# Kernel tuning notes

Hardware: AMD Instinct MI355X
Metric: run time of the kernel (lower is better)

## Reference

```python
import jax, jax.numpy as jnp
import numpy as np

B, L, D = 4, 2048, 1024
E, K, H = 8, 2, 4096
EPS = 1e-5


def setup_inputs() -> dict:
    key = jax.random.key(0)
    ks = jax.random.split(key, 6)
    x = jax.random.normal(ks[0], (B, L, D), jnp.float32)
    gate_w = jax.random.normal(ks[1], (E, D), jnp.float32) * 0.02
    W1 = jax.random.normal(ks[2], (E, D, H), jnp.float32) * 0.02
    b1 = jnp.zeros((E, H), jnp.float32)
    W2 = jax.random.normal(ks[3], (E, H, D), jnp.float32) * 0.02
    b2 = jnp.zeros((E, D), jnp.float32)
    gamma = jnp.ones((D,), jnp.float32)
    beta = jnp.zeros((D,), jnp.float32)
    return {"x": x, "gamma": gamma, "beta": beta, "gate_w": gate_w,
            "W1": W1, "b1": b1, "W2": W2, "b2": b2}


def reference(x, gamma, beta, gate_w, W1, b1, W2, b2):
    # LayerNorm (biased variance, eps=1e-5, matches torch.nn.LayerNorm)
    mu = jnp.mean(x, axis=-1, keepdims=True)
    var = jnp.mean((x - mu) ** 2, axis=-1, keepdims=True)
    xn = (x - mu) / jnp.sqrt(var + EPS) * gamma + beta
    xf = xn.reshape(-1, D)  # (T, D), T = B*L
    T = xf.shape[0]

    # gating: top-k logits -> softmax -> scatter into dense gates (T, E)
    logits = xf @ gate_w.T  # (T, E)
    top_v, top_i = jax.lax.top_k(logits, K)
    top_g = jax.nn.softmax(top_v, axis=-1)
    gates = jnp.zeros_like(logits).at[jnp.arange(T)[:, None], top_i].set(top_g)

    # experts: dense-equivalent of masked gather/FFN/scatter-add combine.
    # Non-selected experts contribute with gate weight 0 -> identical math.
    h = jax.nn.gelu(jnp.einsum('td,edh->teh', xf, W1) + b1, approximate=False)
    y = jnp.einsum('teh,ehd->ted', h, W2) + b2  # (T, E, D)
    out = jnp.einsum('te,ted->td', gates, y).reshape(B, L, D) + x

    # load-balance loss: MSE(mean gate per expert, uniform)
    load = jnp.mean(gates, axis=0)
    bal_loss = jnp.mean((load - 1.0 / E) ** 2)
    return out, bal_loss
```

## Files before the change

kernel.cpp:

```cpp
#include <hip/hip_runtime.h>
#include <hip/hip_bf16.h>

#define T_TOK 8192
#define DD 1024
#define EE 8
#define HH 4096
#define NA (2 * T_TOK)
#define NBLK (NA / 256)

typedef __bf16 bf16_t;
typedef __bf16 bf16x8 __attribute__((ext_vector_type(8)));
typedef __bf16 bf16x4 __attribute__((ext_vector_type(4)));
typedef float f32x4 __attribute__((ext_vector_type(4)));
typedef int   i32x4 __attribute__((ext_vector_type(4)));

union frag_u { i32x4 i; bf16x8 b; };

#define GLDS(g, l) __builtin_amdgcn_global_load_lds( \
    (const __attribute__((address_space(1))) void*)(g), \
    (__attribute__((address_space(3))) void*)(l), 16, 0, 0)

#define DSR(d, a)      asm volatile("ds_read_b128 %0, %1"           : "=v"(d) : "v"(a))
#define DSRO(d, a, O)  asm volatile("ds_read_b128 %0, %1 offset:" O : "=v"(d) : "v"(a))

#define VMW(N) asm volatile("s_waitcnt vmcnt(" #N ")" ::: "memory")

__device__ __forceinline__ float gelu_fast(float v) {
    float u = v * (0.79788456080286536f + 0.035677408136300125f * v * v);
    float a = 2.8853900817779268f * u;
    a = fminf(fmaxf(a, -87.0f), 87.0f);
    float t = __builtin_amdgcn_exp2f(a);
    return v * t * __builtin_amdgcn_rcpf(t + 1.0f);
}

__global__ __launch_bounds__(256) void ln_gate_kernel(
    const float* __restrict__ x, const float* __restrict__ gamma,
    const float* __restrict__ beta, const float* __restrict__ gate_w,
    bf16_t* __restrict__ xn, int* __restrict__ tokexp, float* __restrict__ tokgate)
{
    const int t = blockIdx.x;
    const int tid = threadIdx.x;
    const int lane = tid & 63, wave = tid >> 6;
    __shared__ float wred[4];
    __shared__ float stats[2];
    __shared__ float lred[32];
    __shared__ float logitsS[8];

    float4 v = ((const float4*)(x + (size_t)t * DD))[tid];
    float s = v.x + v.y + v.z + v.w;
#pragma unroll
    for (int o = 32; o > 0; o >>= 1) s += __shfl_down(s, o, 64);
    if (lane == 0) wred[wave] = s;
    __syncthreads();
    if (tid == 0) stats[0] = (wred[0] + wred[1] + wred[2] + wred[3]) * (1.0f / DD);
    __syncthreads();
    const float mu = stats[0];
    float d0 = v.x - mu, d1 = v.y - mu, d2 = v.z - mu, d3 = v.w - mu;
    float q = d0*d0 + d1*d1 + d2*d2 + d3*d3;
#pragma unroll
    for (int o = 32; o > 0; o >>= 1) q += __shfl_down(q, o, 64);
    __syncthreads();
    if (lane == 0) wred[wave] = q;
    __syncthreads();
    if (tid == 0) stats[1] = rsqrtf((wred[0]+wred[1]+wred[2]+wred[3]) * (1.0f / DD) + 1e-5f);
    __syncthreads();
    const float rstd = stats[1];
    float4 g4 = ((const float4*)gamma)[tid];
    float4 b4 = ((const float4*)beta)[tid];
    float n0 = d0 * rstd * g4.x + b4.x;
    float n1 = d1 * rstd * g4.y + b4.y;
    float n2 = d2 * rstd * g4.z + b4.z;
    float n3 = d3 * rstd * g4.w + b4.w;
    bf16x4 pk = { (bf16_t)n0, (bf16_t)n1, (bf16_t)n2, (bf16_t)n3 };
    ((bf16x4*)(xn + (size_t)t * DD))[tid] = pk;

    float part[8];
#pragma unroll
    for (int e = 0; e < 8; ++e) {
        float4 gw = ((const float4*)(gate_w + (size_t)e * DD))[tid];
        part[e] = n0 * gw.x + n1 * gw.y + n2 * gw.z + n3 * gw.w;
    }
#pragma unroll
    for (int e = 0; e < 8; ++e) {
        float p = part[e];
#pragma unroll
        for (int o = 32; o > 0; o >>= 1) p += __shfl_down(p, o, 64);
        if (lane == 0) lred[wave * 8 + e] = p;
    }
    __syncthreads();
    if (tid < 8) logitsS[tid] = lred[tid] + lred[8 + tid] + lred[16 + tid] + lred[24 + tid];
    __syncthreads();
    if (tid == 0) {
        float best = -1e30f; int e0 = 0;
        for (int e = 0; e < 8; ++e) { float le = logitsS[e]; if (le > best) { best = le; e0 = e; } }
        float best2 = -1e30f; int e1 = (e0 == 0) ? 1 : 0;
        for (int e = 0; e < 8; ++e) if (e != e0) { float le = logitsS[e]; if (le > best2) { best2 = le; e1 = e; } }
        float z = expf(best2 - best);
        float g0 = 1.0f / (1.0f + z);
        float g1 = z * g0;
        tokexp[2*t] = e0; tokexp[2*t+1] = e1;
        tokgate[2*t] = g0; tokgate[2*t+1] = g1;
    }
}

__global__ __launch_bounds__(256) void hist_kernel(
    const int* __restrict__ tokexp, const float* __restrict__ tokgate,
    int* __restrict__ blockcnt, float* __restrict__ blockgsum)
{
    __shared__ int hcnt[EE];
    __shared__ float hg[EE];
    const int b = blockIdx.x, tid = threadIdx.x;
    if (tid < EE) { hcnt[tid] = 0; hg[tid] = 0.f; }
    __syncthreads();
    int idx = b * 256 + tid;
    int e = tokexp[idx];
    atomicAdd(&hcnt[e], 1);
    atomicAdd(&hg[e], tokgate[idx]);
    __syncthreads();
    if (tid < EE) {
        blockcnt[b * EE + tid] = hcnt[tid];
        blockgsum[b * EE + tid] = hg[tid];
    }
}

__global__ __launch_bounds__(64) void offs_bal_kernel(
    const int* __restrict__ blockcnt, const float* __restrict__ blockgsum,
    int* __restrict__ cnt, int* __restrict__ offs, int* __restrict__ basep,
    float* __restrict__ bal_out)
{
    __shared__ int cntS[EE];
    const int tid = threadIdx.x;
    if (tid < EE) {
        int run = 0;
        for (int b = 0; b < NBLK; ++b) {
            basep[b * EE + tid] = run;
            run += blockcnt[b * EE + tid];
        }
        cnt[tid] = run;
        cntS[tid] = run;
    }
    __syncthreads();
    __shared__ int offsS[EE];
    if (tid == 0) {
        int run = 0; 
        for (int e = 0; e < EE; ++e) { offsS[e] = run; offs[e] = run; run += cntS[e]; }
        float bal = 0.f;
        for (int e = 0; e < EE; ++e) {
            float g = 0.f;
            for (int b = 0; b < NBLK; ++b) g += blockgsum[b * EE + e];
            float l = g * (1.0f / T_TOK) - (1.0f / EE);
            bal += l * l;
        }
        bal_out[0] = bal * (1.0f / EE);
    }
    __syncthreads();
    if (tid < EE) {
        for (int b = 0; b < NBLK; ++b) basep[b * EE + tid] += offsS[tid];
    }
}

__global__ __launch_bounds__(256) void scatter_kernel(
    const int* __restrict__ tokexp, const float* __restrict__ tokgate,
    const int* __restrict__ basep,
    int* __restrict__ tok, float* __restrict__ gatev, int* __restrict__ a_of_t)
{
    __shared__ int hcnt[EE];
    const int b = blockIdx.x, tid = threadIdx.x;
    if (tid < EE) hcnt[tid] = 0;
    __syncthreads();
    int idx = b * 256 + tid;
    int e = tokexp[idx];
    int r = atomicAdd(&hcnt[e], 1);
    int a = basep[b * EE + e] + r;
    tok[a] = idx >> 1;
    gatev[a] = tokgate[idx];
    a_of_t[idx] = a;
}

__global__ __launch_bounds__(256) void convT_kernel(
    const float* __restrict__ in, bf16_t* __restrict__ out, int R, int C)
{
    __shared__ float tile[64][65];
    int e = blockIdx.z;
    int c0 = blockIdx.x * 64, r0 = blockIdx.y * 64;
    int tx = threadIdx.x & 63, ty = threadIdx.x >> 6;
    const float* src = in + ((size_t)e * R + r0) * C + c0;
#pragma unroll
    for (int i = 0; i < 16; ++i) {
        int r = ty + i * 4;
        tile[r][tx] = src[(size_t)r * C + tx];
    }
    __syncthreads();
    bf16_t* dst = out + ((size_t)e * C + c0) * R + r0;
#pragma unroll
    for (int i = 0; i < 16; ++i) {
        int cc = ty + i * 4;
        dst[(size_t)cc * R + tx] = (bf16_t)tile[tx][cc];
    }
}


#define MM(tf, nf) \
    acc[tf][nf] = __builtin_amdgcn_mfma_f32_16x16x32_bf16(bB[(nf)&1][0].b, aA[(tf)&3][0].b, acc[tf][nf], 0,0,0); \
    acc[tf][nf] = __builtin_amdgcn_mfma_f32_16x16x32_bf16(bB[(nf)&1][1].b, aA[(tf)&3][1].b, acc[tf][nf], 0,0,0);

#define MFMA16(mq, nq) \
    MM((mq)*4+0, (nq)*2+0) MM((mq)*4+0, (nq)*2+1) \
    MM((mq)*4+1, (nq)*2+0) MM((mq)*4+1, (nq)*2+1) \
    MM((mq)*4+2, (nq)*2+0) MM((mq)*4+2, (nq)*2+1) \
    MM((mq)*4+3, (nq)*2+0) MM((mq)*4+3, (nq)*2+1)

#define LOAD_A(mq_) do { \
    uint32_t a0_ = abase0 + rb + (mq_)*8192u; \
    uint32_t a1_ = abase1 + rb + (mq_)*8192u; \
    DSR (aA[0][0].i, a0_); DSRO(aA[1][0].i, a0_, "2048"); \
    DSRO(aA[2][0].i, a0_, "4096"); DSRO(aA[3][0].i, a0_, "6144"); \
    DSR (aA[0][1].i, a1_); DSRO(aA[1][1].i, a1_, "2048"); \
    DSRO(aA[2][1].i, a1_, "4096"); DSRO(aA[3][1].i, a1_, "6144"); \
} while (0)

#define LOAD_B(nq_) do { \
    uint32_t b0_ = bbase0 + rb + (nq_)*32768u; \
    uint32_t b1_ = bbase1 + rb + (nq_)*32768u; \
    DSR (bB[0][0].i, b0_); DSRO(bB[1][0].i, b0_, "2048"); \
    DSR (bB[0][1].i, b1_); DSRO(bB[1][1].i, b1_, "2048"); \
} while (0)

#define PHASE_MID() do { \
    __builtin_amdgcn_s_barrier(); \
    asm volatile("s_waitcnt lgkmcnt(0)" ::: "memory"); \
    __builtin_amdgcn_sched_barrier(0); \
    __builtin_amdgcn_s_setprio(1); \
} while (0)

#define PHASE_END() do { \
    __builtin_amdgcn_s_setprio(0); \
    __builtin_amdgcn_s_barrier(); \
} while (0)

template<int NT>
__device__ __forceinline__ void mfma_mainloop(
    const bf16_t* pa0, const bf16_t* pa1, const bf16_t* pa2, const bf16_t* pa3,
    const bf16_t* pb0, const bf16_t* pb1, const bf16_t* pb2, const bf16_t* pb3,
    bf16_t* S, f32x4 (&acc)[8][4])
{
    const int tid = threadIdx.x;
    const int lane = tid & 63, wave = tid >> 6;
    const int wm = wave >> 2, wn = wave & 3;
    const int l15 = lane & 15, lq = lane >> 4, rx = l15 & 7;
    const uint32_t csb0 = (uint32_t)((lq ^ rx) * 16);
    const uint32_t csb1 = (uint32_t)(((4 + lq) ^ rx) * 16);
    const uint32_t sbase = (uint32_t)(size_t)(__attribute__((address_space(3))) bf16_t*)S;
    const uint32_t abase0 = sbase + (uint32_t)wm*32768u + (uint32_t)l15*128u + csb0;
    const uint32_t abase1 = sbase + (uint32_t)wm*32768u + (uint32_t)l15*128u + csb1;
    const uint32_t bbase0 = sbase + 16384u + (uint32_t)wn*4096u + (uint32_t)l15*128u + csb0;
    const uint32_t bbase1 = sbase + 16384u + (uint32_t)wn*4096u + (uint32_t)l15*128u + csb1;

    frag_u aA[4][2];
    frag_u bB[2][2];

    {
        bf16_t* wb = S;
        GLDS(pa0, wb +     0 + tid*8); pa0 += 64;
        GLDS(pa2, wb + 16384 + tid*8); pa2 += 64;
        GLDS(pb0, wb +  8192 + tid*8); pb0 += 64;
        GLDS(pb1, wb + 12288 + tid*8); pb1 += 64;
        GLDS(pa1, wb +  4096 + tid*8); pa1 += 64;
        GLDS(pa3, wb + 20480 + tid*8); pa3 += 64;
        GLDS(pb2, wb + 24576 + tid*8); pb2 += 64;
        GLDS(pb3, wb + 28672 + tid*8); pb3 += 64;
    }
    VMW(4);
    __builtin_amdgcn_s_barrier();

    for (int kt = 0; kt < NT; ++kt) {
        const uint32_t rb = (uint32_t)(kt & 1) * 65536u;
        bf16_t* wb = S + (size_t)(((kt + 1) & 1)) * 32768;
        const bool more = (kt + 1 < NT);

        LOAD_A(0); LOAD_B(0);
        if (more) {
            GLDS(pa0, wb +     0 + tid*8); pa0 += 64;
            GLDS(pa2, wb + 16384 + tid*8); pa2 += 64;
            VMW(4);
        } else VMW(2);
        PHASE_MID();
        MFMA16(0, 0)
        PHASE_END();

        LOAD_A(1);
        if (more) {
            GLDS(pb0, wb +  8192 + tid*8); pb0 += 64;
            GLDS(pb1, wb + 12288 + tid*8); pb1 += 64;
            VMW(4);
        } else VMW(0);
        PHASE_MID();
        MFMA16(1, 0)
        PHASE_END();

        LOAD_B(1);
        if (more) {
            GLDS(pa1, wb +  4096 + tid*8); pa1 += 64;
            GLDS(pa3, wb + 20480 + tid*8); pa3 += 64;
            VMW(4);
        }
        PHASE_MID();
        MFMA16(1, 1)
        PHASE_END();

        LOAD_A(0);
        if (more) {
            GLDS(pb2, wb + 24576 + tid*8); pb2 += 64;
            GLDS(pb3, wb + 28672 + tid*8); pb3 += 64;
            VMW(4);
        }
        PHASE_MID();
        MFMA16(0, 1)
        PHASE_END();
    }
}

__global__ __launch_bounds__(512, 2) void ffn1_kernel(
    const bf16_t* __restrict__ xn, const bf16_t* __restrict__ w1t,
    const float* __restrict__ b1, const int* __restrict__ tok,
    const int* __restrict__ cnt, const int* __restrict__ offs,
    bf16_t* __restrict__ h1)
{
    const int e = blockIdx.z;
    const int c = cnt[e];
    const int m0 = blockIdx.y * 256;
    if (m0 >= c) return;
    const int n0 = blockIdx.x * 256;
    const int off = offs[e];

    __shared__ __align__(16) bf16_t S[2 * 4 * 8192];

    const int tid = threadIdx.x;
    const int rloc = tid >> 3;
    const int qx8 = ((tid & 7) ^ (rloc & 7)) * 8;

    int mA0 = m0 + rloc;        if (mA0 >= c) mA0 = c - 1;
    int mA1 = m0 + 64 + rloc;   if (mA1 >= c) mA1 = c - 1;
    int mA2 = m0 + 128 + rloc;  if (mA2 >= c) mA2 = c - 1;
    int mA3 = m0 + 192 + rloc;  if (mA3 >= c) mA3 = c - 1;
    const bf16_t* pa0 = xn + (size_t)tok[off + mA0] * DD + qx8;
    const bf16_t* pa1 = xn + (size_t)tok[off + mA1] * DD + qx8;
    const bf16_t* pa2 = xn + (size_t)tok[off + mA2] * DD + qx8;
    const bf16_t* pa3 = xn + (size_t)tok[off + mA3] * DD + qx8;
    const bf16_t* pb0 = w1t + ((size_t)e * HH + n0 + rloc) * DD + qx8;
    const bf16_t* pb1 = pb0 + (size_t)64 * DD;
    const bf16_t* pb2 = pb0 + (size_t)128 * DD;
    const bf16_t* pb3 = pb0 + (size_t)192 * DD;

    f32x4 acc[8][4] = {};
    mfma_mainloop<DD / 64>(pa0, pa1, pa2, pa3, pb0, pb1, pb2, pb3, S, acc);

    const int lane = tid & 63, wave = tid >> 6;
    const int wm = wave >> 2, wn = wave & 3;
    const int l15 = lane & 15, lq = lane >> 4;

    const float* b1e = b1 + (size_t)e * HH;
#pragma unroll
    for (int tf = 0; tf < 8; ++tf) {
        int m = m0 + wm * 128 + tf * 16 + l15;
        if (m < c) {
            bf16_t* hrow = h1 + (size_t)(off + m) * HH;
#pragma unroll
            for (int nf = 0; nf < 4; ++nf) {
                int n = n0 + (nf >> 1) * 128 + wn * 32 + (nf & 1) * 16 + lq * 4;
                float4 bb = *(const float4*)(b1e + n);
                f32x4 a = acc[tf][nf];
                bf16x4 pk;
                pk[0] = (bf16_t)gelu_fast(a[0] + bb.x);
                pk[1] = (bf16_t)gelu_fast(a[1] + bb.y);
                pk[2] = (bf16_t)gelu_fast(a[2] + bb.z);
                pk[3] = (bf16_t)gelu_fast(a[3] + bb.w);
                *(bf16x4*)(hrow + n) = pk;
            }
        }
    }
}

__global__ __launch_bounds__(512, 2) void ffn2_kernel(
    const bf16_t* __restrict__ h1, const bf16_t* __restrict__ w2t,
    const float* __restrict__ b2, const float* __restrict__ gatev,
    const int* __restrict__ cnt, const int* __restrict__ offs,
    bf16_t* __restrict__ yv)
{
    const int e = blockIdx.z;
    const int c = cnt[e];
    const int m0 = blockIdx.y * 256;
    if (m0 >= c) return;
    const int n0 = blockIdx.x * 256;
    const int off = offs[e];

    __shared__ __align__(16) bf16_t S[2 * 4 * 8192];

    const int tid = threadIdx.x;
    const int rloc = tid >> 3;
    const int qx8 = ((tid & 7) ^ (rloc & 7)) * 8;

    int mA0 = m0 + rloc;        if (mA0 >= c) mA0 = c - 1;
    int mA1 = m0 + 64 + rloc;   if (mA1 >= c) mA1 = c - 1;
    int mA2 = m0 + 128 + rloc;  if (mA2 >= c) mA2 = c - 1;
    int mA3 = m0 + 192 + rloc;  if (mA3 >= c) mA3 = c - 1;
    const bf16_t* pa0 = h1 + (size_t)(off + mA0) * HH + qx8;
    const bf16_t* pa1 = h1 + (size_t)(off + mA1) * HH + qx8;
    const bf16_t* pa2 = h1 + (size_t)(off + mA2) * HH + qx8;
    const bf16_t* pa3 = h1 + (size_t)(off + mA3) * HH + qx8;
    const bf16_t* pb0 = w2t + ((size_t)e * DD + n0 + rloc) * HH + qx8;
    const bf16_t* pb1 = pb0 + (size_t)64 * HH;
    const bf16_t* pb2 = pb0 + (size_t)128 * HH;
    const bf16_t* pb3 = pb0 + (size_t)192 * HH;

    f32x4 acc[8][4] = {};
    mfma_mainloop<HH / 64>(pa0, pa1, pa2, pa3, pb0, pb1, pb2, pb3, S, acc);

    const int lane = tid & 63, wave = tid >> 6;
    const int wm = wave >> 2, wn = wave & 3;
    const int l15 = lane & 15, lq = lane >> 4;

    const float* b2e = b2 + (size_t)e * DD;
#pragma unroll
    for (int tf = 0; tf < 8; ++tf) {
        int m = m0 + wm * 128 + tf * 16 + l15;
        if (m < c) {
            float g = gatev[off + m];
            bf16_t* yrow = yv + (size_t)(off + m) * DD;
#pragma unroll
            for (int nf = 0; nf < 4; ++nf) {
                int n = n0 + (nf >> 1) * 128 + wn * 32 + (nf & 1) * 16 + lq * 4;
                float4 bb = *(const float4*)(b2e + n);
                f32x4 a = acc[tf][nf];
                bf16x4 pk;
                pk[0] = (bf16_t)((a[0] + bb.x) * g);
                pk[1] = (bf16_t)((a[1] + bb.y) * g);
                pk[2] = (bf16_t)((a[2] + bb.z) * g);
                pk[3] = (bf16_t)((a[3] + bb.w) * g);
                *(bf16x4*)(yrow + n) = pk;
            }
        }
    }
}

__global__ __launch_bounds__(256) void combine_kernel(
    const float* __restrict__ x, const bf16_t* __restrict__ yv,
    const int* __restrict__ a_of_t, float* __restrict__ outp)
{
    int t = blockIdx.x;
    int tid = threadIdx.x;
    int a0 = a_of_t[2*t], a1 = a_of_t[2*t+1];
    float4 xv = ((const float4*)(x + (size_t)t * DD))[tid];
    bf16x4 y0 = ((const bf16x4*)(yv + (size_t)a0 * DD))[tid];
    bf16x4 y1 = ((const bf16x4*)(yv + (size_t)a1 * DD))[tid];
    float4 o;
    o.x = xv.x + (float)y0[0] + (float)y1[0];
    o.y = xv.y + (float)y0[1] + (float)y1[1];
    o.z = xv.z + (float)y0[2] + (float)y1[2];
    o.w = xv.w + (float)y0[3] + (float)y1[3];
    ((float4*)(outp + (size_t)t * DD))[tid] = o;
}

extern "C" void kernel_launch(void* const* d_in, const int* in_sizes, int n_in,
                              void* d_out, int out_size, void* d_ws, size_t ws_size,
                              hipStream_t stream)
{
    const float* x      = (const float*)d_in[0];
    const float* gamma  = (const float*)d_in[1];
    const float* beta   = (const float*)d_in[2];
    const float* gate_w = (const float*)d_in[3];
    const float* W1     = (const float*)d_in[4];
    const float* b1     = (const float*)d_in[5];
    const float* W2     = (const float*)d_in[6];
    const float* b2     = (const float*)d_in[7];
    float* outp = (float*)d_out;
    float* bal_out = outp + (size_t)T_TOK * DD;

    char* ws = (char*)d_ws;
    size_t off = 0;
    auto alloc = [&](size_t bytes) {
        char* p = ws + off;
        off += (bytes + 255) & ~(size_t)255;
        return p;
    };
    bf16_t* xn   = (bf16_t*)alloc((size_t)T_TOK * DD * 2);
    bf16_t* w1t  = (bf16_t*)alloc((size_t)EE * HH * DD * 2);
    bf16_t* w2t  = (bf16_t*)alloc((size_t)EE * DD * HH * 2);
    bf16_t* h1   = (bf16_t*)alloc((size_t)NA * HH * 2);
    bf16_t* yv   = (bf16_t*)alloc((size_t)NA * DD * 2);
    int*   tok     = (int*)alloc(NA * 4);
    float* gatev   = (float*)alloc(NA * 4);
    int*   a_of_t  = (int*)alloc(NA * 4);
    int*   tokexp  = (int*)alloc(NA * 4);
    float* tokgate = (float*)alloc(NA * 4);
    int*   blockcnt  = (int*)alloc(NBLK * EE * 4);
    float* blockgsum = (float*)alloc(NBLK * EE * 4);
    int*   basep     = (int*)alloc(NBLK * EE * 4);
    int*   cnt  = (int*)alloc(EE * 4);
    int*   offs = (int*)alloc(EE * 4);

    convT_kernel<<<dim3(HH/64, DD/64, EE), 256, 0, stream>>>(W1, w1t, DD, HH);
    convT_kernel<<<dim3(DD/64, HH/64, EE), 256, 0, stream>>>(W2, w2t, HH, DD);
    ln_gate_kernel<<<T_TOK, 256, 0, stream>>>(x, gamma, beta, gate_w, xn, tokexp, tokgate);
    hist_kernel<<<NBLK, 256, 0, stream>>>(tokexp, tokgate, blockcnt, blockgsum);
    offs_bal_kernel<<<1, 64, 0, stream>>>(blockcnt, blockgsum, cnt, offs, basep, bal_out);
    scatter_kernel<<<NBLK, 256, 0, stream>>>(tokexp, tokgate, basep, tok, gatev, a_of_t);
    ffn1_kernel<<<dim3(HH/256, 32, EE), 512, 0, stream>>>(xn, w1t, b1, tok, cnt, offs, h1);
    ffn2_kernel<<<dim3(DD/256, 32, EE), 512, 0, stream>>>(h1, w2t, b2, gatev, cnt, offs, yv);
    combine_kernel<<<T_TOK, 256, 0, stream>>>(x, yv, a_of_t, outp);
}
```

Measured before the change: 781.7 us.

## Restructure MFMA main loop to one barrier per k-tile with finer LDS waits

The GEMM main loop is rescheduled so that every global-to-LDS load for the next k-tile is issued together. There is now a single vmcnt(0) wait plus one barrier per iteration, where before there were four phases, each with two barriers. All four B fragments are held in registers, and the MFMA blocks are split on partial lgkmcnt waits so compute can start before every LDS read has landed. The goal is to cut barrier and synchronisation overhead. The cost is more VGPR pressure and less slack for hiding global-load latency, since the loads must complete within one k-tile of compute.

New measurement: 754.4 us. -3.5%, faster.

```diff
diff --git a/kernel.cpp b/kernel.cpp
--- a/kernel.cpp
+++ b/kernel.cpp
@@ -23,7 +23,9 @@
 #define DSR(d, a)      asm volatile("ds_read_b128 %0, %1"           : "=v"(d) : "v"(a))
 #define DSRO(d, a, O)  asm volatile("ds_read_b128 %0, %1 offset:" O : "=v"(d) : "v"(a))
 
-#define VMW(N) asm volatile("s_waitcnt vmcnt(" #N ")" ::: "memory")
+#define VMW(N)  asm volatile("s_waitcnt vmcnt(" #N ")" ::: "memory")
+#define LGK(N)  do { asm volatile("s_waitcnt lgkmcnt(" #N ")" ::: "memory"); \
+                     __builtin_amdgcn_sched_barrier(0); } while (0)
 
 __device__ __forceinline__ float gelu_fast(float v) {
     float u = v * (0.79788456080286536f + 0.035677408136300125f * v * v);
@@ -200,42 +202,26 @@
 }
 
 
-#define MM(tf, nf) \
-    acc[tf][nf] = __builtin_amdgcn_mfma_f32_16x16x32_bf16(bB[(nf)&1][0].b, aA[(tf)&3][0].b, acc[tf][nf], 0,0,0); \
-    acc[tf][nf] = __builtin_amdgcn_mfma_f32_16x16x32_bf16(bB[(nf)&1][1].b, aA[(tf)&3][1].b, acc[tf][nf], 0,0,0);
-
-#define MFMA16(mq, nq) \
-    MM((mq)*4+0, (nq)*2+0) MM((mq)*4+0, (nq)*2+1) \
-    MM((mq)*4+1, (nq)*2+0) MM((mq)*4+1, (nq)*2+1) \
-    MM((mq)*4+2, (nq)*2+0) MM((mq)*4+2, (nq)*2+1) \
-    MM((mq)*4+3, (nq)*2+0) MM((mq)*4+3, (nq)*2+1)
-
-#define LOAD_A(mq_) do { \
+#define MMC(tf, nf) \
+    acc[tf][nf] = __builtin_amdgcn_mfma_f32_16x16x32_bf16(bF[nf][0].b, aF[(tf)&3][0].b, acc[tf][nf], 0,0,0); \
+    acc[tf][nf] = __builtin_amdgcn_mfma_f32_16x16x32_bf16(bF[nf][1].b, aF[(tf)&3][1].b, acc[tf][nf], 0,0,0);
+
+#define LOAD_A_P(mq_) do { \
     uint32_t a0_ = abase0 + rb + (mq_)*8192u; \
     uint32_t a1_ = abase1 + rb + (mq_)*8192u; \
-    DSR (aA[0][0].i, a0_); DSRO(aA[1][0].i, a0_, "2048"); \
-    DSRO(aA[2][0].i, a0_, "4096"); DSRO(aA[3][0].i, a0_, "6144"); \
-    DSR (aA[0][1].i, a1_); DSRO(aA[1][1].i, a1_, "2048"); \
-    DSRO(aA[2][1].i, a1_, "4096"); DSRO(aA[3][1].i, a1_, "6144"); \
+    DSR (aF[0][0].i, a0_);         DSR (aF[0][1].i, a1_); \
+    DSRO(aF[1][0].i, a0_, "2048"); DSRO(aF[1][1].i, a1_, "2048"); \
+    DSRO(aF[2][0].i, a0_, "4096"); DSRO(aF[2][1].i, a1_, "4096"); \
+    DSRO(aF[3][0].i, a0_, "6144"); DSRO(aF[3][1].i, a1_, "6144"); \
 } while (0)
 
-#define LOAD_B(nq_) do { \
-    uint32_t b0_ = bbase0 + rb + (nq_)*32768u; \
-    uint32_t b1_ = bbase1 + rb + (nq_)*32768u; \
-    DSR (bB[0][0].i, b0_); DSRO(bB[1][0].i, b0_, "2048"); \
-    DSR (bB[0][1].i, b1_); DSRO(bB[1][1].i, b1_, "2048"); \
-} while (0)
-
-#define PHASE_MID() do { \
-    __builtin_amdgcn_s_barrier(); \
-    asm volatile("s_waitcnt lgkmcnt(0)" ::: "memory"); \
-    __builtin_amdgcn_sched_barrier(0); \
-    __builtin_amdgcn_s_setprio(1); \
-} while (0)
-
-#define PHASE_END() do { \
-    __builtin_amdgcn_s_setprio(0); \
-    __builtin_amdgcn_s_barrier(); \
+#define LOAD_B_ALL() do { \
+    uint32_t l0 = bbase0 + rb; \
+    uint32_t l1 = bbase1 + rb; \
+    DSR (bF[0][0].i, l0);           DSRO(bF[1][0].i, l0, "2048"); \
+    DSR (bF[0][1].i, l1);           DSRO(bF[1][1].i, l1, "2048"); \
+    DSRO(bF[2][0].i, l0, "32768");  DSRO(bF[3][0].i, l0, "34816"); \
+    DSRO(bF[2][1].i, l1, "32768");  DSRO(bF[3][1].i, l1, "34816"); \
 } while (0)
 
 template<int NT>
@@ -256,67 +242,68 @@
     const uint32_t bbase0 = sbase + 16384u + (uint32_t)wn*4096u + (uint32_t)l15*128u + csb0;
     const uint32_t bbase1 = sbase + 16384u + (uint32_t)wn*4096u + (uint32_t)l15*128u + csb1;
 
-    frag_u aA[4][2];
-    frag_u bB[2][2];
+    frag_u aF[4][2];
+    frag_u bF[4][2];
 
     {
         bf16_t* wb = S;
         GLDS(pa0, wb +     0 + tid*8); pa0 += 64;
+        GLDS(pa1, wb +  4096 + tid*8); pa1 += 64;
         GLDS(pa2, wb + 16384 + tid*8); pa2 += 64;
+        GLDS(pa3, wb + 20480 + tid*8); pa3 += 64;
         GLDS(pb0, wb +  8192 + tid*8); pb0 += 64;
         GLDS(pb1, wb + 12288 + tid*8); pb1 += 64;
-        GLDS(pa1, wb +  4096 + tid*8); pa1 += 64;
-        GLDS(pa3, wb + 20480 + tid*8); pa3 += 64;
         GLDS(pb2, wb + 24576 + tid*8); pb2 += 64;
         GLDS(pb3, wb + 28672 + tid*8); pb3 += 64;
     }
-    VMW(4);
-    __builtin_amdgcn_s_barrier();
 
     for (int kt = 0; kt < NT; ++kt) {
         const uint32_t rb = (uint32_t)(kt & 1) * 65536u;
-        bf16_t* wb = S + (size_t)(((kt + 1) & 1)) * 32768;
+        bf16_t* wb = S + (size_t)((kt + 1) & 1) * 32768;
         const bool more = (kt + 1 < NT);
 
-        LOAD_A(0); LOAD_B(0);
+        VMW(0);
+        __builtin_amdgcn_s_barrier();
+
+        LOAD_A_P(0);
+        LOAD_B_ALL();
+
         if (more) {
             GLDS(pa0, wb +     0 + tid*8); pa0 += 64;
+            GLDS(pa1, wb +  4096 + tid*8); pa1 += 64;
             GLDS(pa2, wb + 16384 + tid*8); pa2 += 64;
-            VMW(4);
-        } else VMW(2);
-        PHASE_MID();
-        MFMA16(0, 0)
-        PHASE_END();
-
-        LOAD_A(1);
-        if (more) {
+            GLDS(pa3, wb + 20480 + tid*8); pa3 += 64;
             GLDS(pb0, wb +  8192 + tid*8); pb0 += 64;
             GLDS(pb1, wb + 12288 + tid*8); pb1 += 64;
-            VMW(4);
-        } else VMW(0);
-        PHASE_MID();
-        MFMA16(1, 0)
-        PHASE_END();
-
-        LOAD_B(1);
-        if (more) {
-            GLDS(pa1, wb +  4096 + tid*8); pa1 += 64;
-            GLDS(pa3, wb + 20480 + tid*8); pa3 += 64;
-            VMW(4);
-        }
-        PHASE_MID();
-        MFMA16(1, 1)
-        PHASE_END();
-
-        LOAD_A(0);
-        if (more) {
             GLDS(pb2, wb + 24576 + tid*8); pb2 += 64;
             GLDS(pb3, wb + 28672 + tid*8); pb3 += 64;
-            VMW(4);
         }
-        PHASE_MID();
-        MFMA16(0, 1)
-        PHASE_END();
+
+        LGK(4);
+        __builtin_amdgcn_s_setprio(1);
+        MMC(0,0) MMC(1,0) MMC(2,0) MMC(3,0)
+        MMC(0,1) MMC(1,1) MMC(2,1) MMC(3,1)
+        __builtin_amdgcn_s_setprio(0);
+
+        LGK(0);
+        __builtin_amdgcn_s_setprio(1);
+        MMC(0,2) MMC(1,2) MMC(2,2) MMC(3,2)
+        MMC(0,3) MMC(1,3) MMC(2,3) MMC(3,3)
+        __builtin_amdgcn_s_setprio(0);
+
+        LOAD_A_P(1);
+
+        LGK(4);
+        __builtin_amdgcn_s_setprio(1);
+        MMC(4,0) MMC(4,1) MMC(4,2) MMC(4,3)
+        MMC(5,0) MMC(5,1) MMC(5,2) MMC(5,3)
+        __builtin_amdgcn_s_setprio(0);
+
+        LGK(0);
+        __builtin_amdgcn_s_setprio(1);
+        MMC(6,0) MMC(6,1) MMC(6,2) MMC(6,3)
+        MMC(7,0) MMC(7,1) MMC(7,2) MMC(7,3)
+        __builtin_amdgcn_s_setprio(0);
     }
 }
 
```
